# Performance work log

Measured on AMD Instinct MI355X. Metric: run time of the kernel, lower is better.

## Reference

```python
import jax, jax.numpy as jnp
import numpy as np

B, T, D, H = 256, 1024, 128, 256
SHIFT = 1


def setup_inputs() -> dict:
    key = jax.random.key(0)
    ks = jax.random.split(key, 16)

    def w(k, shp):
        return jax.random.normal(k, shp, dtype=jnp.float32) / np.float32(np.sqrt(shp[0]))

    return {
        "x": jax.random.normal(ks[0], (B, T, D), dtype=jnp.float32),
        "Wx": w(ks[1], (D, H)), "bx": jnp.zeros((H,), jnp.float32),
        "W1": w(ks[2], (D, 100)), "b1": jnp.zeros((100,), jnp.float32),
        "W2": w(ks[3], (100, 100)), "b2": jnp.zeros((100,), jnp.float32),
        "W3": w(ks[4], (100, 100)), "b3": jnp.zeros((100,), jnp.float32),
        "W4": w(ks[5], (100, 50)), "b4": jnp.zeros((50,), jnp.float32),
        "W5": w(ks[6], (50, H)), "b5": jnp.zeros((H,), jnp.float32),
        "Wo": w(ks[7], (H, 1)), "bo": jnp.zeros((1,), jnp.float32),
        "shift": SHIFT,
    }


def reference(x, Wx, bx, W1, b1, W2, b2, W3, b3, W4, b4, W5, b5, Wo, bo, shift):
    # x: [B, T, D] -> time-major [T, B, D] (matches input.permute(1,0,2))
    xs = jnp.swapaxes(x, 0, 1)
    # Input-dependent parts are independent of hidden state: batch them over time.
    lin_x = xs @ Wx + bx                       # [T, B, H]
    h = jax.nn.relu(xs @ W1 + b1)
    h = jax.nn.relu(h @ W2 + b2)
    h = jax.nn.relu(h @ W3 + b3)
    h = jax.nn.relu(h @ W4 + b4)
    fx = jax.nn.sigmoid(h @ W5 + b5)           # [T, B, H]
    gate = fx * jax.nn.sigmoid(lin_x)          # [T, B, H]

    def step(hid, bt):
        hid = jax.nn.relu(jnp.roll(hid, shift, axis=-1) + bt)
        return hid, None

    hidden0 = jnp.zeros((x.shape[0], Wx.shape[1]), dtype=x.dtype)
    hidden, _ = jax.lax.scan(step, hidden0, gate)
    output = jax.nn.sigmoid(hidden @ Wo + bo)  # [B, 1]
    return (output, hidden)
```

## Files before the change

### kernel.cpp

```cpp
#include <hip/hip_runtime.h>
#include <math.h>

#define B_N 256
#define T_N 1024
#define D_N 128
#define H_N 256

#define SXS 136
#define SPS 120
#define SWS 136
#define SW5 72

#define SWX_OFF 0
#define SP_OFF  15232
#define SQ_OFF  22912
#define GUARD   30592
#define ACC_OFF 30600
#define SMEM_SH 31112

typedef __attribute__((ext_vector_type(8))) short short8;
typedef __attribute__((ext_vector_type(4))) float f32x4;

#define WXT_OFF 0
#define W1T_OFF 32768
#define W2T_OFF 47104
#define W3T_OFF 61440
#define W4T_OFF 75776
#define W5T_OFF 83968
#define WT_TOTAL 100352

__device__ __forceinline__ float sigmoid_f(float z) {
    return 1.0f / (1.0f + __expf(-z));
}
__device__ __forceinline__ unsigned short f2bf(float f) {
    unsigned u = __float_as_uint(f);
    return (unsigned short)((u + 0x7FFFu + ((u >> 16) & 1u)) >> 16);
}

__global__ __launch_bounds__(256) void prep_weights(
    const float* __restrict__ Wx, const float* __restrict__ W1,
    const float* __restrict__ W2, const float* __restrict__ W3,
    const float* __restrict__ W4, const float* __restrict__ W5,
    short* __restrict__ wt)
{
    int idx = blockIdx.x * 256 + threadIdx.x;
    if (idx >= WT_TOTAL) return;
    const float* src; int Kp, K, N, local;
    if (idx < W1T_OFF)      { src = Wx; Kp = 128; K = 128; N = 256; local = idx - WXT_OFF; }
    else if (idx < W2T_OFF) { src = W1; Kp = 128; K = 128; N = 100; local = idx - W1T_OFF; }
    else if (idx < W3T_OFF) { src = W2; Kp = 128; K = 100; N = 100; local = idx - W2T_OFF; }
    else if (idx < W4T_OFF) { src = W3; Kp = 128; K = 100; N = 100; local = idx - W3T_OFF; }
    else if (idx < W5T_OFF) { src = W4; Kp = 128; K = 100; N =  50; local = idx - W4T_OFF; }
    else                    { src = W5; Kp =  64; K =  50; N = 256; local = idx - W5T_OFF; }
    int n = local / Kp, k = local % Kp;
    float v = (k < K && n < N) ? src[(size_t)k * N + n] : 0.0f;
    wt[idx] = (short)f2bf(v);
}

template<int NR, int KP, int STR>
__device__ __forceinline__ void coop_load(const short* __restrict__ g,
                                          short* __restrict__ dst, int tid)
{
    constexpr int SPR = KP / 8;
    constexpr int TOT = NR * SPR;
    #pragma unroll
    for (int i = 0; i < TOT / 256; ++i) {
        const int sl = tid + i * 256;
        const int r  = sl / SPR;
        const int c  = sl & (SPR - 1);
        *reinterpret_cast<short8*>(dst + r * STR + c * 8) =
            *reinterpret_cast<const short8*>(g + (size_t)r * KP + c * 8);
    }
}

template<int STRIDE>
__device__ __forceinline__ void loadA(const short* __restrict__ base, short8 (&a)[4],
                                      int mbase, int lr, int lq)
{
    #pragma unroll
    for (int k = 0; k < 4; ++k)
        a[k] = *reinterpret_cast<const short8*>(&base[(mbase + lr) * STRIDE + k * 32 + lq * 8]);
}

template<int NT, int OUTS>
__device__ __forceinline__ void denseL(const short8 (&a)[4], const short* __restrict__ sW,
                                       const float* __restrict__ bias, int ncap,
                                       short* __restrict__ dst, int mbase, int lr, int lq)
{
    #pragma unroll 2
    for (int nt = 0; nt < NT; ++nt) {
        const int n0 = nt * 16;
        f32x4 acc = {0.f, 0.f, 0.f, 0.f};
        #pragma unroll
        for (int k = 0; k < 4; ++k) {
            const short8 bf = *reinterpret_cast<const short8*>(&sW[(n0 + lr) * SWS + k * 32 + lq * 8]);
            acc = __builtin_amdgcn_mfma_f32_16x16x32_bf16(a[k], bf, acc, 0, 0, 0);
        }
        const bool valid = (n0 + lr < ncap);
        const float bv = valid ? bias[n0 + lr] : 0.0f;
        #pragma unroll
        for (int r = 0; r < 4; ++r) {
            float v = valid ? fmaxf(acc[r] + bv, 0.0f) : 0.0f;
            dst[(mbase + lq * 4 + r) * OUTS + n0 + lr] = (short)f2bf(v);
        }
    }
}

__global__ __launch_bounds__(256, 2) void srnn_gate_scan(
    const float* __restrict__ x, const short* __restrict__ wt,
    const float* __restrict__ bx, const float* __restrict__ b1,
    const float* __restrict__ b2, const float* __restrict__ b3,
    const float* __restrict__ b4, const float* __restrict__ b5,
    const int* __restrict__ shiftp,
    float* __restrict__ out)
{
    __shared__ __align__(16) short smem[SMEM_SH];
    short* sWX = smem + SWX_OFF;
    short* sP  = smem + SP_OFF;
    short* sQ  = smem + SQ_OFF;
    float* accum = reinterpret_cast<float*>(smem + ACC_OFF);

    const int tid  = threadIdx.x;
    const int b    = blockIdx.x & 255;
    const int seg  = blockIdx.x >> 8;
    const int lane = tid & 63;
    const int mbase = (tid >> 6) * 16;
    const int lr = lane & 15;
    const int lq = lane >> 4;
    const int s  = *shiftp;
    const int tw0 = seg * 64 + mbase;

    {
        const float4 z = {0.f, 0.f, 0.f, 0.f};
        float4* dst = reinterpret_cast<float4*>(smem + SP_OFF);
        #pragma unroll
        for (int i = 0; i < 8; ++i) {
            int sl = tid + i * 256;
            if (sl < (SMEM_SH - SP_OFF) / 8) dst[sl] = z;
        }
    }

    {
        const float* xsrc = x + ((size_t)b * T_N + tw0) * D_N;
        #pragma unroll
        for (int it = 0; it < 8; ++it) {
            const int row = (lane >> 5) + it * 2;
            const int col = (lane & 31) * 4;
            float4 v = *reinterpret_cast<const float4*>(&xsrc[row * D_N + col]);
            uint2 p;
            p.x = (unsigned)f2bf(v.x) | ((unsigned)f2bf(v.y) << 16);
            p.y = (unsigned)f2bf(v.z) | ((unsigned)f2bf(v.w) << 16);
            *reinterpret_cast<uint2*>(&sWX[(mbase + row) * SXS + col]) = p;
        }
    }
    short8 ax4[4];
    loadA<SXS>(sWX, ax4, mbase, lr, lq);
    __syncthreads();

    short8 aL[4];
    coop_load<112, 128, SWS>(wt + W1T_OFF, sWX, tid);
    __syncthreads();
    denseL<7, SPS>(ax4, sWX, b1, 100, sP, mbase, lr, lq);
    __syncthreads();
    coop_load<112, 128, SWS>(wt + W2T_OFF, sWX, tid);
    loadA<SPS>(sP, aL, mbase, lr, lq);
    __syncthreads();
    denseL<7, SPS>(aL, sWX, b2, 100, sQ, mbase, lr, lq);
    __syncthreads();
    coop_load<112, 128, SWS>(wt + W3T_OFF, sWX, tid);
    loadA<SPS>(sQ, aL, mbase, lr, lq);
    __syncthreads();
    denseL<7, SPS>(aL, sWX, b3, 100, sP, mbase, lr, lq);
    __syncthreads();
    coop_load<64, 128, SWS>(wt + W4T_OFF, sWX, tid);
    loadA<SPS>(sP, aL, mbase, lr, lq);
    __syncthreads();
    denseL<4, SPS>(aL, sWX, b4, 50, sQ, mbase, lr, lq);
    __syncthreads();

    short8 c0, c1;
    c0 = *reinterpret_cast<const short8*>(&sQ[(mbase + lr) * SPS + 0 + lq * 8]);
    c1 = *reinterpret_cast<const short8*>(&sQ[(mbase + lr) * SPS + 32 + lq * 8]);
    short* sW5s = sWX + 8704;
    for (int ch = 0; ch < 4; ++ch) {
        coop_load<64, 128, SWS>(wt + WXT_OFF + ch * 64 * 128, sWX, tid);
        coop_load<64, 64, SW5>(wt + W5T_OFF + ch * 64 * 64, sW5s, tid);
        __syncthreads();
        #pragma unroll 2
        for (int ntl = 0; ntl < 4; ++ntl) {
            const int n0  = ntl * 16;
            const int gn0 = ch * 64 + n0;
            f32x4 axv = {0.f, 0.f, 0.f, 0.f};
            #pragma unroll
            for (int k = 0; k < 4; ++k) {
                const short8 bf = *reinterpret_cast<const short8*>(&sWX[(n0 + lr) * SWS + k * 32 + lq * 8]);
                axv = __builtin_amdgcn_mfma_f32_16x16x32_bf16(ax4[k], bf, axv, 0, 0, 0);
            }
            f32x4 a5v = {0.f, 0.f, 0.f, 0.f};
            {
                const short8 bf0 = *reinterpret_cast<const short8*>(&sW5s[(n0 + lr) * SW5 + 0 + lq * 8]);
                const short8 bf1 = *reinterpret_cast<const short8*>(&sW5s[(n0 + lr) * SW5 + 32 + lq * 8]);
                a5v = __builtin_amdgcn_mfma_f32_16x16x32_bf16(c0, bf0, a5v, 0, 0, 0);
                a5v = __builtin_amdgcn_mfma_f32_16x16x32_bf16(c1, bf1, a5v, 0, 0, 0);
            }
            const float bxv = bx[gn0 + lr];
            const float b5v = b5[gn0 + lr];
            #pragma unroll
            for (int r = 0; r < 4; ++r) {
                const int t = tw0 + lq * 4 + r;
                const float g = sigmoid_f(a5v[r] + b5v) * sigmoid_f(axv[r] + bxv);
                int v = gn0 + lr + s * (T_N - 1 - t);
                v %= H_N; if (v < 0) v += H_N;
                atomicAdd(&accum[v], g);
            }
        }
        __syncthreads();
    }

    atomicAdd(&out[256 + b * 256 + tid], accum[tid]);
}

__global__ __launch_bounds__(256) void srnn_output(
    const float* __restrict__ Wo, const float* __restrict__ bo,
    float* __restrict__ out)
{
    __shared__ float red[256];
    const int b = blockIdx.x, tid = threadIdx.x;
    red[tid] = out[256 + b * 256 + tid] * Wo[tid];
    __syncthreads();
    #pragma unroll
    for (int off = 128; off > 0; off >>= 1) {
        if (tid < off) red[tid] += red[tid + off];
        __syncthreads();
    }
    if (tid == 0) out[b] = sigmoid_f(red[0] + bo[0]);
}

extern "C" void kernel_launch(void* const* d_in, const int* in_sizes, int n_in,
                              void* d_out, int out_size, void* d_ws, size_t ws_size,
                              hipStream_t stream)
{
    const float* x  = (const float*)d_in[0];
    const float* Wx = (const float*)d_in[1];
    const float* bx = (const float*)d_in[2];
    const float* W1 = (const float*)d_in[3];
    const float* b1 = (const float*)d_in[4];
    const float* W2 = (const float*)d_in[5];
    const float* b2 = (const float*)d_in[6];
    const float* W3 = (const float*)d_in[7];
    const float* b3 = (const float*)d_in[8];
    const float* W4 = (const float*)d_in[9];
    const float* b4 = (const float*)d_in[10];
    const float* W5 = (const float*)d_in[11];
    const float* b5 = (const float*)d_in[12];
    const float* Wo = (const float*)d_in[13];
    const float* bo = (const float*)d_in[14];
    const int* shiftp = (const int*)d_in[15];
    float* out = (float*)d_out;
    short* wt  = (short*)d_ws;

    hipMemsetAsync(d_out, 0, (size_t)out_size * sizeof(float), stream);

    prep_weights<<<dim3((WT_TOTAL + 255) / 256), dim3(256), 0, stream>>>(
        Wx, W1, W2, W3, W4, W5, wt);
    srnn_gate_scan<<<dim3(4096), dim3(256), 0, stream>>>(
        x, wt, bx, b1, b2, b3, b4, b5, shiftp, out);
    srnn_output<<<dim3(256), dim3(256), 0, stream>>>(Wo, bo, out);
}
```

Before: 653.9 us.

## Read MFMA-fragment-packed weights straight from global, drop LDS weight staging

```diff
diff --git a/kernel.cpp b/kernel.cpp
--- a/kernel.cpp
+++ b/kernel.cpp
@@ -6,17 +6,13 @@
 #define D_N 128
 #define H_N 256
 
-#define SXS 136
 #define SPS 120
-#define SWS 136
-#define SW5 72
-
-#define SWX_OFF 0
-#define SP_OFF  15232
-#define SQ_OFF  22912
-#define GUARD   30592
-#define ACC_OFF 30600
-#define SMEM_SH 31112
+
+#define SP_OFF  0
+#define SQ_OFF  7680
+#define GUARD_OFF 15360
+#define ACC_OFF 15368
+#define SMEM_SH 15880
 
 typedef __attribute__((ext_vector_type(8))) short short8;
 typedef __attribute__((ext_vector_type(4))) float f32x4;
@@ -45,32 +41,24 @@
 {
     int idx = blockIdx.x * 256 + threadIdx.x;
     if (idx >= WT_TOTAL) return;
-    const float* src; int Kp, K, N, local;
-    if (idx < W1T_OFF)      { src = Wx; Kp = 128; K = 128; N = 256; local = idx - WXT_OFF; }
-    else if (idx < W2T_OFF) { src = W1; Kp = 128; K = 128; N = 100; local = idx - W1T_OFF; }
-    else if (idx < W3T_OFF) { src = W2; Kp = 128; K = 100; N = 100; local = idx - W2T_OFF; }
-    else if (idx < W4T_OFF) { src = W3; Kp = 128; K = 100; N = 100; local = idx - W3T_OFF; }
-    else if (idx < W5T_OFF) { src = W4; Kp = 128; K = 100; N =  50; local = idx - W4T_OFF; }
-    else                    { src = W5; Kp =  64; K =  50; N = 256; local = idx - W5T_OFF; }
-    int n = local / Kp, k = local % Kp;
+    const float* src; int base, KR, K, N;
+    if (idx < W1T_OFF)      { src = Wx; base = WXT_OFF; KR = 4; K = 128; N = 256; }
+    else if (idx < W2T_OFF) { src = W1; base = W1T_OFF; KR = 4; K = 128; N = 100; }
+    else if (idx < W3T_OFF) { src = W2; base = W2T_OFF; KR = 4; K = 100; N = 100; }
+    else if (idx < W4T_OFF) { src = W3; base = W3T_OFF; KR = 4; K = 100; N = 100; }
+    else if (idx < W5T_OFF) { src = W4; base = W4T_OFF; KR = 4; K = 100; N =  50; }
+    else                    { src = W5; base = W5T_OFF; KR = 2; K =  50; N = 256; }
+    int e    = idx - base;
+    int j    = e & 7;
+    int slot = e >> 3;
+    int lane = slot & 63;
+    int kk   = slot >> 6;
+    int k4   = kk & (KR - 1);
+    int nt   = kk / KR;
+    int n = nt * 16 + (lane & 15);
+    int k = k4 * 32 + (lane >> 4) * 8 + j;
     float v = (k < K && n < N) ? src[(size_t)k * N + n] : 0.0f;
     wt[idx] = (short)f2bf(v);
-}
-
-template<int NR, int KP, int STR>
-__device__ __forceinline__ void coop_load(const short* __restrict__ g,
-                                          short* __restrict__ dst, int tid)
-{
-    constexpr int SPR = KP / 8;
-    constexpr int TOT = NR * SPR;
-    #pragma unroll
-    for (int i = 0; i < TOT / 256; ++i) {
-        const int sl = tid + i * 256;
-        const int r  = sl / SPR;
-        const int c  = sl & (SPR - 1);
-        *reinterpret_cast<short8*>(dst + r * STR + c * 8) =
-            *reinterpret_cast<const short8*>(g + (size_t)r * KP + c * 8);
-    }
 }
 
 template<int STRIDE>
@@ -83,9 +71,10 @@
 }
 
 template<int NT, int OUTS>
-__device__ __forceinline__ void denseL(const short8 (&a)[4], const short* __restrict__ sW,
-                                       const float* __restrict__ bias, int ncap,
-                                       short* __restrict__ dst, int mbase, int lr, int lq)
+__device__ __forceinline__ void denseLG(const short8 (&a)[4], const short* __restrict__ gW,
+                                        const float* __restrict__ bias, int ncap,
+                                        short* __restrict__ dst, int mbase, int lr, int lq,
+                                        int lane)
 {
     #pragma unroll 2
     for (int nt = 0; nt < NT; ++nt) {
@@ -93,7 +82,7 @@
         f32x4 acc = {0.f, 0.f, 0.f, 0.f};
         #pragma unroll
         for (int k = 0; k < 4; ++k) {
-            const short8 bf = *reinterpret_cast<const short8*>(&sW[(n0 + lr) * SWS + k * 32 + lq * 8]);
+            const short8 bf = *reinterpret_cast<const short8*>(&gW[((nt * 4 + k) * 64 + lane) * 8]);
             acc = __builtin_amdgcn_mfma_f32_16x16x32_bf16(a[k], bf, acc, 0, 0, 0);
         }
         const bool valid = (n0 + lr < ncap);
@@ -106,7 +95,7 @@
     }
 }
 
-__global__ __launch_bounds__(256, 2) void srnn_gate_scan(
+__global__ __launch_bounds__(256, 4) void srnn_gate_scan(
     const float* __restrict__ x, const short* __restrict__ wt,
     const float* __restrict__ bx, const float* __restrict__ b1,
     const float* __restrict__ b2, const float* __restrict__ b3,
@@ -115,9 +104,8 @@
     float* __restrict__ out)
 {
     __shared__ __align__(16) short smem[SMEM_SH];
-    short* sWX = smem + SWX_OFF;
-    short* sP  = smem + SP_OFF;
-    short* sQ  = smem + SQ_OFF;
+    short* sP = smem + SP_OFF;
+    short* sQ = smem + SQ_OFF;
     float* accum = reinterpret_cast<float*>(smem + ACC_OFF);
 
     const int tid  = threadIdx.x;
@@ -132,90 +120,73 @@
 
     {
         const float4 z = {0.f, 0.f, 0.f, 0.f};
-        float4* dst = reinterpret_cast<float4*>(smem + SP_OFF);
+        float4* dst = reinterpret_cast<float4*>(smem);
         #pragma unroll
         for (int i = 0; i < 8; ++i) {
             int sl = tid + i * 256;
-            if (sl < (SMEM_SH - SP_OFF) / 8) dst[sl] = z;
-        }
-    }
-
+            if (sl < SMEM_SH / 8) dst[sl] = z;
+        }
+    }
+
+    short8 ax4[4];
     {
-        const float* xsrc = x + ((size_t)b * T_N + tw0) * D_N;
-        #pragma unroll
-        for (int it = 0; it < 8; ++it) {
-            const int row = (lane >> 5) + it * 2;
-            const int col = (lane & 31) * 4;
-            float4 v = *reinterpret_cast<const float4*>(&xsrc[row * D_N + col]);
-            uint2 p;
-            p.x = (unsigned)f2bf(v.x) | ((unsigned)f2bf(v.y) << 16);
-            p.y = (unsigned)f2bf(v.z) | ((unsigned)f2bf(v.w) << 16);
-            *reinterpret_cast<uint2*>(&sWX[(mbase + row) * SXS + col]) = p;
-        }
-    }
-    short8 ax4[4];
-    loadA<SXS>(sWX, ax4, mbase, lr, lq);
+        const float* xr = x + ((size_t)b * T_N + tw0 + lr) * D_N;
+        #pragma unroll
+        for (int k = 0; k < 4; ++k) {
+            const float4 v0 = *reinterpret_cast<const float4*>(&xr[k * 32 + lq * 8]);
+            const float4 v1 = *reinterpret_cast<const float4*>(&xr[k * 32 + lq * 8 + 4]);
+            short8 t;
+            t[0] = (short)f2bf(v0.x); t[1] = (short)f2bf(v0.y);
+            t[2] = (short)f2bf(v0.z); t[3] = (short)f2bf(v0.w);
+            t[4] = (short)f2bf(v1.x); t[5] = (short)f2bf(v1.y);
+            t[6] = (short)f2bf(v1.z); t[7] = (short)f2bf(v1.w);
+            ax4[k] = t;
+        }
+    }
     __syncthreads();
 
     short8 aL[4];
-    coop_load<112, 128, SWS>(wt + W1T_OFF, sWX, tid);
+    denseLG<7, SPS>(ax4, wt + W1T_OFF, b1, 100, sP, mbase, lr, lq, lane);
+    loadA<SPS>(sP, aL, mbase, lr, lq);
+    denseLG<7, SPS>(aL, wt + W2T_OFF, b2, 100, sQ, mbase, lr, lq, lane);
+    loadA<SPS>(sQ, aL, mbase, lr, lq);
+    denseLG<7, SPS>(aL, wt + W3T_OFF, b3, 100, sP, mbase, lr, lq, lane);
+    loadA<SPS>(sP, aL, mbase, lr, lq);
+    denseLG<4, SPS>(aL, wt + W4T_OFF, b4, 50, sQ, mbase, lr, lq, lane);
+
+    short8 c0 = *reinterpret_cast<const short8*>(&sQ[(mbase + lr) * SPS + 0 + lq * 8]);
+    short8 c1 = *reinterpret_cast<const short8*>(&sQ[(mbase + lr) * SPS + 32 + lq * 8]);
+
+    const short* gWx = wt + WXT_OFF;
+    const short* gW5 = wt + W5T_OFF;
+    #pragma unroll 2
+    for (int ntl = 0; ntl < 16; ++ntl) {
+        const int n0 = ntl * 16;
+        f32x4 axv = {0.f, 0.f, 0.f, 0.f};
+        #pragma unroll
+        for (int k = 0; k < 4; ++k) {
+            const short8 bf = *reinterpret_cast<const short8*>(&gWx[((ntl * 4 + k) * 64 + lane) * 8]);
+            axv = __builtin_amdgcn_mfma_f32_16x16x32_bf16(ax4[k], bf, axv, 0, 0, 0);
+        }
+        f32x4 a5v = {0.f, 0.f, 0.f, 0.f};
+        {
+            const short8 bf0 = *reinterpret_cast<const short8*>(&gW5[((ntl * 2 + 0) * 64 + lane) * 8]);
+            const short8 bf1 = *reinterpret_cast<const short8*>(&gW5[((ntl * 2 + 1) * 64 + lane) * 8]);
+            a5v = __builtin_amdgcn_mfma_f32_16x16x32_bf16(c0, bf0, a5v, 0, 0, 0);
+            a5v = __builtin_amdgcn_mfma_f32_16x16x32_bf16(c1, bf1, a5v, 0, 0, 0);
+        }
+        const float bxv = bx[n0 + lr];
+        const float b5v = b5[n0 + lr];
+        #pragma unroll
+        for (int r = 0; r < 4; ++r) {
+            const int t = tw0 + lq * 4 + r;
+            const float g = sigmoid_f(a5v[r] + b5v) * sigmoid_f(axv[r] + bxv);
+            int v = n0 + lr + s * (T_N - 1 - t);
+            v %= H_N; if (v < 0) v += H_N;
+            atomicAdd(&accum[v], g);
+        }
+    }
     __syncthreads();
-    denseL<7, SPS>(ax4, sWX, b1, 100, sP, mbase, lr, lq);
-    __syncthreads();
-    coop_load<112, 128, SWS>(wt + W2T_OFF, sWX, tid);
-    loadA<SPS>(sP, aL, mbase, lr, lq);
-    __syncthreads();
-    denseL<7, SPS>(aL, sWX, b2, 100, sQ, mbase, lr, lq);
-    __syncthreads();
-    coop_load<112, 128, SWS>(wt + W3T_OFF, sWX, tid);
-    loadA<SPS>(sQ, aL, mbase, lr, lq);
-    __syncthreads();
-    denseL<7, SPS>(aL, sWX, b3, 100, sP, mbase, lr, lq);
-    __syncthreads();
-    coop_load<64, 128, SWS>(wt + W4T_OFF, sWX, tid);
-    loadA<SPS>(sP, aL, mbase, lr, lq);
-    __syncthreads();
-    denseL<4, SPS>(aL, sWX, b4, 50, sQ, mbase, lr, lq);
-    __syncthreads();
-
-    short8 c0, c1;
-    c0 = *reinterpret_cast<const short8*>(&sQ[(mbase + lr) * SPS + 0 + lq * 8]);
-    c1 = *reinterpret_cast<const short8*>(&sQ[(mbase + lr) * SPS + 32 + lq * 8]);
-    short* sW5s = sWX + 8704;
-    for (int ch = 0; ch < 4; ++ch) {
-        coop_load<64, 128, SWS>(wt + WXT_OFF + ch * 64 * 128, sWX, tid);
-        coop_load<64, 64, SW5>(wt + W5T_OFF + ch * 64 * 64, sW5s, tid);
-        __syncthreads();
-        #pragma unroll 2
-        for (int ntl = 0; ntl < 4; ++ntl) {
-            const int n0  = ntl * 16;
-            const int gn0 = ch * 64 + n0;
-            f32x4 axv = {0.f, 0.f, 0.f, 0.f};
-            #pragma unroll
-            for (int k = 0; k < 4; ++k) {
-                const short8 bf = *reinterpret_cast<const short8*>(&sWX[(n0 + lr) * SWS + k * 32 + lq * 8]);
-                axv = __builtin_amdgcn_mfma_f32_16x16x32_bf16(ax4[k], bf, axv, 0, 0, 0);
-            }
-            f32x4 a5v = {0.f, 0.f, 0.f, 0.f};
-            {
-                const short8 bf0 = *reinterpret_cast<const short8*>(&sW5s[(n0 + lr) * SW5 + 0 + lq * 8]);
-                const short8 bf1 = *reinterpret_cast<const short8*>(&sW5s[(n0 + lr) * SW5 + 32 + lq * 8]);
-                a5v = __builtin_amdgcn_mfma_f32_16x16x32_bf16(c0, bf0, a5v, 0, 0, 0);
-                a5v = __builtin_amdgcn_mfma_f32_16x16x32_bf16(c1, bf1, a5v, 0, 0, 0);
-            }
-            const float bxv = bx[gn0 + lr];
-            const float b5v = b5[gn0 + lr];
-            #pragma unroll
-            for (int r = 0; r < 4; ++r) {
-                const int t = tw0 + lq * 4 + r;
-                const float g = sigmoid_f(a5v[r] + b5v) * sigmoid_f(axv[r] + bxv);
-                int v = gn0 + lr + s * (T_N - 1 - t);
-                v %= H_N; if (v < 0) v += H_N;
-                atomicAdd(&accum[v], g);
-            }
-        }
-        __syncthreads();
-    }
 
     atomicAdd(&out[256 + b * 256 + tid], accum[tid]);
 }
```

Measured after the change: 576.5 us. 11.8% less time.
